# Kernel tuning notes

Measured on AMD Instinct MI355X. Metric: run time of the kernel, lower is better.

The kernel has to match this reference:

```python
import jax, jax.numpy as jnp
import numpy as np

NUM_ITERS = 3
NUM_SLOTS = 8
D = 128
MLP_HIDDEN = 128
EPS = 1e-8
LN_EPS = 1e-5
B, N = 64, 4096


def _layer_norm(x, g, b):
    m = jnp.mean(x, axis=-1, keepdims=True)
    v = jnp.mean(jnp.square(x - m), axis=-1, keepdims=True)
    return (x - m) * jax.lax.rsqrt(v + LN_EPS) * g + b


def setup_inputs() -> dict:
    key = jax.random.key(0)
    ks = jax.random.split(key, 16)
    s = 1.0 / np.sqrt(D)
    inp = {
        "x": jax.random.normal(ks[0], (B, N, D), jnp.float32),
        "slots_init": jax.random.normal(ks[1], (B, NUM_SLOTS, D), jnp.float32),
        "Wq": jax.random.normal(ks[2], (D, D), jnp.float32) * s,
        "bq": jnp.zeros((D,), jnp.float32),
        "Wk": jax.random.normal(ks[3], (D, D), jnp.float32) * s,
        "bk": jnp.zeros((D,), jnp.float32),
        "Wv": jax.random.normal(ks[4], (D, D), jnp.float32) * s,
        "bv": jnp.zeros((D,), jnp.float32),
        "g_in": jnp.ones((D,), jnp.float32), "b_in": jnp.zeros((D,), jnp.float32),
        "g_slot": jnp.ones((D,), jnp.float32), "b_slot": jnp.zeros((D,), jnp.float32),
        "g_mlp": jnp.ones((D,), jnp.float32), "b_mlp": jnp.zeros((D,), jnp.float32),
        "W1": jax.random.normal(ks[5], (MLP_HIDDEN, D), jnp.float32) * s,
        "b1": jnp.zeros((MLP_HIDDEN,), jnp.float32),
        "W2": jax.random.normal(ks[6], (D, MLP_HIDDEN), jnp.float32) * (1.0 / np.sqrt(MLP_HIDDEN)),
        "b2": jnp.zeros((D,), jnp.float32),
        "W_ih": jax.random.normal(ks[7], (3 * D, D), jnp.float32) * s,
        "W_hh": jax.random.normal(ks[8], (3 * D, D), jnp.float32) * s,
        "b_ih": jnp.zeros((3 * D,), jnp.float32),
        "b_hh": jnp.zeros((3 * D,), jnp.float32),
    }
    return inp


def _gru_cell(x, h, W_ih, W_hh, b_ih, b_hh):
    # torch.nn.GRUCell semantics
    gi = x @ W_ih.T + b_ih          # [.., 3D]
    gh = h @ W_hh.T + b_hh
    i_r, i_z, i_n = jnp.split(gi, 3, axis=-1)
    h_r, h_z, h_n = jnp.split(gh, 3, axis=-1)
    r = jax.nn.sigmoid(i_r + h_r)
    z = jax.nn.sigmoid(i_z + h_z)
    n = jnp.tanh(i_n + r * h_n)
    return (1.0 - z) * n + z * h


def reference(x, slots_init, Wq, bq, Wk, bk, Wv, bv, g_in, b_in, g_slot, b_slot,
              g_mlp, b_mlp, W1, b1, W2, b2, W_ih, W_hh, b_ih, b_hh):
    xn = _layer_norm(x, g_in, b_in)                 # [B,N,D]
    keys = xn @ Wk.T + bk                            # [B,N,D]
    values = xn @ Wv.T + bv                          # [B,N,D]
    scale = D ** -0.5
    slots = slots_init                               # [B,K,D]
    for _ in range(NUM_ITERS):
        prev = slots
        s = _layer_norm(slots, g_slot, b_slot)
        q = s @ Wq.T + bq                            # [B,K,D]
        logits = jnp.einsum('bid,bkd->bik', q, keys) * scale  # [B,K,N]
        attn = jax.nn.softmax(logits, axis=1)        # softmax over SLOT axis
        attn = attn + EPS
        attn = attn / jnp.sum(attn, axis=-1, keepdims=True)
        updates = jnp.einsum('bkd,bik->bid', values, attn)     # [B,K,D]
        slots = _gru_cell(updates.reshape(-1, D), prev.reshape(-1, D),
                          W_ih, W_hh, b_ih, b_hh).reshape(x.shape[0], -1, D)
        h = jax.nn.relu(_layer_norm(slots, g_mlp, b_mlp) @ W1.T + b1)
        slots = slots + (h @ W2.T + b2)
    return slots
```

## Files before the change

### kernel.cpp

```cpp
#include <hip/hip_runtime.h>
#include <hip/hip_bf16.h>

#define B_ 64
#define N_ 4096
#define KS 8
#define NCH 32
#define NG 2
#define TP 136
#define LNEPS 1e-5f
#define EPSA 1e-8f
#define SCALE 0.08838834764831845f

typedef short short8  __attribute__((ext_vector_type(8)));
typedef short short4v __attribute__((ext_vector_type(4)));
typedef float f32x4   __attribute__((ext_vector_type(4)));

__device__ __forceinline__ unsigned short f2bf(float f) {
  union { float f; unsigned u; } v; v.f = f;
  unsigned r = v.u + 0x7fffu + ((v.u >> 16) & 1u);
  return (unsigned short)(r >> 16);
}
__device__ __forceinline__ float bflo(unsigned u) {
  union { unsigned u; float f; } c; c.u = u << 16; return c.f;
}
__device__ __forceinline__ float bfhi(unsigned u) {
  union { unsigned u; float f; } c; c.u = u & 0xffff0000u; return c.f;
}
__device__ __forceinline__ float sigmf(float x) { return 1.f / (1.f + __expf(-x)); }

__global__ __launch_bounds__(256) void prep_weights(
    const float* __restrict__ Wih, const float* __restrict__ Whh,
    const float* __restrict__ Wq,  const float* __restrict__ Wv,
    const float* __restrict__ W1,  const float* __restrict__ W2,
    float* __restrict__ WgT, float* __restrict__ WqT,
    float* __restrict__ WvT, float* __restrict__ W1T, float* __restrict__ W2T)
{
  int id = blockIdx.x * 256 + threadIdx.x;
  if (id < 98304) {
    int d = id / 768, j = id % 768;
    WgT[id] = (j < 384) ? Wih[j*128 + d] : Whh[(j-384)*128 + d];
  } else if (id < 114688) {
    int k = id - 98304; WqT[k] = Wq[(k % 128) * 128 + k / 128];
  } else if (id < 131072) {
    int k = id - 114688; WvT[k] = Wv[(k % 128) * 128 + k / 128];
  } else if (id < 147456) {
    int k = id - 131072; W1T[k] = W1[(k % 128) * 128 + k / 128];
  } else if (id < 163840) {
    int k = id - 147456; W2T[k] = W2[(k % 128) * 128 + k / 128];
  }
}

__global__ __launch_bounds__(256) void q_init_kernel(
    const float* __restrict__ slots_in, const float* __restrict__ g_slot, const float* __restrict__ b_slot,
    const float* __restrict__ WqT, const float* __restrict__ bq,
    const float* __restrict__ Wk, const float* __restrict__ bk,
    float* __restrict__ qt, float* __restrict__ qc)
{
  __shared__ float sarr[128];
  __shared__ float qarr[128];
  int row = blockIdx.x, t = threadIdx.x;
  if (t < 64) {
    float a = slots_in[row*128 + t], b = slots_in[row*128 + 64 + t];
    float s = a + b, s2 = a*a + b*b;
    #pragma unroll
    for (int st = 1; st < 64; st <<= 1) { s += __shfl_xor(s, st); s2 += __shfl_xor(s2, st); }
    float mean = s * (1.f/128.f);
    float rstd = rsqrtf(s2 * (1.f/128.f) - mean*mean + LNEPS);
    sarr[t]    = (a - mean) * rstd * g_slot[t]    + b_slot[t];
    sarr[t+64] = (b - mean) * rstd * g_slot[t+64] + b_slot[t+64];
  }
  __syncthreads();
  if (t < 128) {
    float a = bq[t];
    for (int d = 0; d < 128; d++) a += sarr[d] * WqT[d*128 + t];
    qarr[t] = a;
  }
  __syncthreads();
  if (t < 128) {
    float a = 0.f;
    for (int j = 0; j < 128; j++) a += qarr[j] * Wk[j*128 + t];
    qt[row*128 + t] = a * SCALE;
  }
  if (t < 64) {
    float c = qarr[t]*bk[t] + qarr[t+64]*bk[t+64];
    #pragma unroll
    for (int st = 1; st < 64; st <<= 1) c += __shfl_xor(c, st);
    if (t == 0) qc[row] = c * SCALE;
  }
}

__global__ __launch_bounds__(256) void ln_kernel(
    const float* __restrict__ x, const float* __restrict__ g_in, const float* __restrict__ b_in,
    unsigned short* __restrict__ xn)
{
  const int tid = threadIdx.x;
  const int w = tid >> 6, lane = tid & 63;
  const int half = lane >> 5, sl = lane & 31;
  const size_t row0 = (size_t)blockIdx.x * 128 + w * 32 + half;

  float4 gg = *(const float4*)(g_in + sl*4);
  float4 bb = *(const float4*)(b_in + sl*4);

  for (int i = 0; i < 16; i++) {
    size_t row = row0 + i*2;
    float4 v = *(const float4*)(x + row*128 + sl*4);
    float s  = v.x + v.y + v.z + v.w;
    float s2 = v.x*v.x + v.y*v.y + v.z*v.z + v.w*v.w;
    #pragma unroll
    for (int st = 1; st < 32; st <<= 1) { s += __shfl_xor(s, st); s2 += __shfl_xor(s2, st); }
    float mean = s * (1.f/128.f);
    float rstd = rsqrtf(s2*(1.f/128.f) - mean*mean + LNEPS);
    unsigned short h0 = f2bf((v.x - mean)*rstd*gg.x + bb.x);
    unsigned short h1 = f2bf((v.y - mean)*rstd*gg.y + bb.y);
    unsigned short h2 = f2bf((v.z - mean)*rstd*gg.z + bb.z);
    unsigned short h3 = f2bf((v.w - mean)*rstd*gg.w + bb.w);
    uint2 pk;
    pk.x = (unsigned)h0 | ((unsigned)h1 << 16);
    pk.y = (unsigned)h2 | ((unsigned)h3 << 16);
    *(uint2*)(xn + row*128 + sl*4) = pk;
  }
}

__global__ __launch_bounds__(256) void attn_kernel(
    unsigned short* __restrict__ xn,
    const float* __restrict__ qt, const float* __restrict__ qc,
    float* __restrict__ Upart, float* __restrict__ Spart)
{
  __shared__ union ShMem {
    unsigned short xt[4][16][TP];
    float ured[4][8][128];
  } sh;
  __shared__ __align__(16) float pb[4][16][8];
  __shared__ float sred[4][8];

  const int tid = threadIdx.x;
  const int w = tid >> 6, lane = tid & 63;
  const int chunk = blockIdx.x, batch = blockIdx.y;
  const int m = lane & 15, quad = lane >> 4;

  short8 afrag[4];
  if (m < KS) {
    const float* qp = qt + (batch*KS + m)*128 + quad*8;
    #pragma unroll
    for (int kc = 0; kc < 4; kc++) {
      short8 a;
      #pragma unroll
      for (int j = 0; j < 8; j++) a[j] = (short)f2bf(qp[kc*32 + j]);
      afrag[kc] = a;
    }
  } else {
    #pragma unroll
    for (int kc = 0; kc < 4; kc++) {
      short8 a;
      #pragma unroll
      for (int j = 0; j < 8; j++) a[j] = 0;
      afrag[kc] = a;
    }
  }
  float creg[4];
  #pragma unroll
  for (int r = 0; r < 4; r++) creg[r] = qc[batch*KS + ((quad*4 + r) & 7)];

  float u0[8], u1[8];
  #pragma unroll
  for (int i = 0; i < 8; i++) { u0[i] = 0.f; u1[i] = 0.f; }
  float sAcc[4] = {0.f, 0.f, 0.f, 0.f};

  for (int g = 0; g < NG; g++) {
    const int tb = ((chunk*4 + w)*NG + g)*16;

    short8 bfrag[4];
    const unsigned short* xp = xn + (size_t)(batch*N_ + tb + m)*128;
    #pragma unroll
    for (int kc = 0; kc < 4; kc++) {
      bfrag[kc] = *(const short8*)(xp + kc*32 + quad*8);
      *(short8*)&sh.xt[w][m][kc*32 + quad*8] = bfrag[kc];
    }

    f32x4 acc = {0.f, 0.f, 0.f, 0.f};
    #pragma unroll
    for (int kc = 0; kc < 4; kc++)
      acc = __builtin_amdgcn_mfma_f32_16x16x32_bf16(afrag[kc], bfrag[kc], acc, 0, 0, 0);
    float l[4], o[4];
    #pragma unroll
    for (int r = 0; r < 4; r++) l[r] = acc[r] + creg[r];
    #pragma unroll
    for (int r = 0; r < 4; r++) o[r] = __shfl_xor(l[r], 16);
    float mx = fmaxf(fmaxf(fmaxf(l[0], l[1]), fmaxf(l[2], l[3])),
                     fmaxf(fmaxf(o[0], o[1]), fmaxf(o[2], o[3])));
    float e0 = __expf(l[0]-mx), e1 = __expf(l[1]-mx), e2 = __expf(l[2]-mx), e3 = __expf(l[3]-mx);
    float den = e0+e1+e2+e3 + __expf(o[0]-mx)+__expf(o[1]-mx)+__expf(o[2]-mx)+__expf(o[3]-mx);
    float rd = 1.f / den;
    float p0 = e0*rd + EPSA, p1 = e1*rd + EPSA, p2 = e2*rd + EPSA, p3 = e3*rd + EPSA;
    if (lane < 32) {
      float4 pv; pv.x = p0; pv.y = p1; pv.z = p2; pv.w = p3;
      *(float4*)&pb[w][m][quad*4] = pv;
    }

    #pragma unroll
    for (int t = 0; t < 16; t++) {
      float4 pA = *(const float4*)&pb[w][t][0];
      float4 pB = *(const float4*)&pb[w][t][4];
      unsigned vp = *(const unsigned*)&sh.xt[w][t][lane*2];
      float f0 = bflo(vp), f1 = bfhi(vp);
      u0[0] += pA.x*f0; u1[0] += pA.x*f1;
      u0[1] += pA.y*f0; u1[1] += pA.y*f1;
      u0[2] += pA.z*f0; u1[2] += pA.z*f1;
      u0[3] += pA.w*f0; u1[3] += pA.w*f1;
      u0[4] += pB.x*f0; u1[4] += pB.x*f1;
      u0[5] += pB.y*f0; u1[5] += pB.y*f1;
      u0[6] += pB.z*f0; u1[6] += pB.z*f1;
      u0[7] += pB.w*f0; u1[7] += pB.w*f1;
    }

    float sac[4] = {p0, p1, p2, p3};
    #pragma unroll
    for (int st = 1; st < 16; st <<= 1) {
      #pragma unroll
      for (int r = 0; r < 4; r++) sac[r] += __shfl_xor(sac[r], st);
    }
    #pragma unroll
    for (int r = 0; r < 4; r++) sAcc[r] += sac[r];
  }

  if (lane == 0)  { sred[w][0]=sAcc[0]; sred[w][1]=sAcc[1]; sred[w][2]=sAcc[2]; sred[w][3]=sAcc[3]; }
  if (lane == 16) { sred[w][4]=sAcc[0]; sred[w][5]=sAcc[1]; sred[w][6]=sAcc[2]; sred[w][7]=sAcc[3]; }

  __syncthreads();
  #pragma unroll
  for (int i = 0; i < 8; i++)
    *(float2*)&sh.ured[w][i][lane*2] = make_float2(u0[i], u1[i]);
  __syncthreads();

  {
    const float* ur = &sh.ured[0][0][0];
    int i4 = tid * 4;
    float4 a = *(const float4*)(ur + i4);
    float4 b = *(const float4*)(ur + 1024 + i4);
    float4 c = *(const float4*)(ur + 2048 + i4);
    float4 d = *(const float4*)(ur + 3072 + i4);
    float4 o4;
    o4.x = a.x+b.x+c.x+d.x; o4.y = a.y+b.y+c.y+d.y;
    o4.z = a.z+b.z+c.z+d.z; o4.w = a.w+b.w+c.w+d.w;
    *(float4*)(Upart + (size_t)(batch*NCH + chunk)*1024 + i4) = o4;
    if (tid < 8)
      Spart[(batch*NCH + chunk)*8 + tid] =
        sred[0][tid] + sred[1][tid] + sred[2][tid] + sred[3][tid];
  }
}

__global__ __launch_bounds__(256) void update_kernel(
    const float* __restrict__ slots_in, float* __restrict__ slots_out,
    const float* __restrict__ Upart, const float* __restrict__ Spart,
    const float* __restrict__ WvT, const float* __restrict__ bv,
    const float* __restrict__ WgT,
    const float* __restrict__ b_ih, const float* __restrict__ b_hh,
    const float* __restrict__ g_mlp, const float* __restrict__ b_mlp,
    const float* __restrict__ W1T, const float* __restrict__ b1,
    const float* __restrict__ W2T, const float* __restrict__ b2,
    const float* __restrict__ g_slot, const float* __restrict__ b_slot,
    const float* __restrict__ WqT, const float* __restrict__ bq,
    const float* __restrict__ Wk, const float* __restrict__ bk,
    float* __restrict__ qt, float* __restrict__ qc)
{
  __shared__ float bu[128], su[128], hb[128];
  __shared__ float gg[768];
  __shared__ float s1[128], smv[128], hmv[128], s2v[128], sqv[128], qa[128];
  __shared__ float up2[2][128];
  __shared__ float stats[2], sSum;
  int row = blockIdx.x, t = threadIdx.x;
  int batch = row >> 3, slot = row & 7;
  const int col = t & 127, hf = t >> 7;

  {
    const float* Up = Upart + ((size_t)(batch*NCH + hf*16)*8 + slot)*128 + col;
    float ua = 0.f;
    #pragma unroll
    for (int c = 0; c < 16; c++) ua += Up[(size_t)c*1024];
    up2[hf][col] = ua;
  }
  if (t < NCH) {
    float sv = Spart[(batch*NCH + t)*8 + slot];
    #pragma unroll
    for (int st = 1; st < NCH; st <<= 1) sv += __shfl_xor(sv, st);
    if (t == 0) sSum = sv;
  }
  if (t >= 64 && t < 192) hb[t-64] = slots_in[row*128 + (t-64)];
  __syncthreads();
  if (t < 128) bu[t] = (up2[0][t] + up2[1][t]) / sSum;
  __syncthreads();
  {
    float a = hf ? 0.f : bv[col];
    const float* W = WvT + hf*64*128;
    const float* v = bu + hf*64;
    #pragma unroll 8
    for (int d = 0; d < 64; d++) a += v[d] * W[d*128 + col];
    __syncthreads();
    up2[hf][col] = a;
  }
  __syncthreads();
  if (t < 128) su[t] = up2[0][t] + up2[1][t];
  __syncthreads();
  {
    float a0 = b_ih[t];
    float a1 = (t < 128) ? b_ih[256+t] : b_hh[t-128];
    float a2 = b_hh[t+128];
    const float* v1p = (t < 128) ? su : hb;
    for (int d = 0; d < 128; d++) {
      float sd = su[d], hd = hb[d], vd = v1p[d];
      const float* wr = WgT + d*768 + t;
      a0 += sd * wr[0];
      a1 += vd * wr[256];
      a2 += hd * wr[512];
    }
    gg[t] = a0; gg[t+256] = a1; gg[t+512] = a2;
  }
  __syncthreads();
  if (t < 128) {
    float r = sigmf(gg[t] + gg[384+t]);
    float z = sigmf(gg[128+t] + gg[512+t]);
    float n = tanhf(gg[256+t] + r * gg[640+t]);
    s1[t] = (1.f - z)*n + z*hb[t];
  }
  __syncthreads();
  if (t < 64) {
    float a = s1[t], b = s1[t+64];
    float s = a + b, s2 = a*a + b*b;
    #pragma unroll
    for (int st = 1; st < 64; st <<= 1) { s += __shfl_xor(s, st); s2 += __shfl_xor(s2, st); }
    if (t == 0) { float mean = s*(1.f/128.f); stats[0] = mean;
                  stats[1] = rsqrtf(s2*(1.f/128.f) - mean*mean + LNEPS); }
  }
  __syncthreads();
  if (t < 128) smv[t] = (s1[t] - stats[0])*stats[1]*g_mlp[t] + b_mlp[t];
  __syncthreads();
  {
    float a = hf ? 0.f : b1[col];
    const float* W = W1T + hf*64*128;
    const float* v = smv + hf*64;
    #pragma unroll 8
    for (int d = 0; d < 64; d++) a += v[d] * W[d*128 + col];
    up2[hf][col] = a;
  }
  __syncthreads();
  if (t < 128) hmv[t] = fmaxf(up2[0][t] + up2[1][t], 0.f);
  __syncthreads();
  {
    float a = 0.f;
    const float* W = W2T + hf*64*128;
    const float* v = hmv + hf*64;
    #pragma unroll 8
    for (int d = 0; d < 64; d++) a += v[d] * W[d*128 + col];
    up2[hf][col] = a;
  }
  __syncthreads();
  if (t < 128) {
    float a = s1[t] + b2[t] + up2[0][t] + up2[1][t];
    s2v[t] = a;
    slots_out[row*128 + t] = a;
  }
  __syncthreads();
  if (t < 64) {
    float a = s2v[t], b = s2v[t+64];
    float s = a + b, s2 = a*a + b*b;
    #pragma unroll
    for (int st = 1; st < 64; st <<= 1) { s += __shfl_xor(s, st); s2 += __shfl_xor(s2, st); }
    if (t == 0) { float mean = s*(1.f/128.f); stats[0] = mean;
                  stats[1] = rsqrtf(s2*(1.f/128.f) - mean*mean + LNEPS); }
  }
  __syncthreads();
  if (t < 128) sqv[t] = (s2v[t] - stats[0])*stats[1]*g_slot[t] + b_slot[t];
  __syncthreads();
  {
    float a = hf ? 0.f : bq[col];
    const float* W = WqT + hf*64*128;
    const float* v = sqv + hf*64;
    #pragma unroll 8
    for (int d = 0; d < 64; d++) a += v[d] * W[d*128 + col];
    up2[hf][col] = a;
  }
  __syncthreads();
  if (t < 128) qa[t] = up2[0][t] + up2[1][t];
  __syncthreads();
  {
    float a = 0.f;
    const float* W = Wk + hf*64*128;
    const float* v = qa + hf*64;
    #pragma unroll 8
    for (int j = 0; j < 64; j++) a += v[j] * W[j*128 + col];
    up2[hf][col] = a;
  }
  __syncthreads();
  if (t < 128) qt[row*128 + t] = (up2[0][t] + up2[1][t]) * SCALE;
  if (t < 64) {
    float c = qa[t]*bk[t] + qa[t+64]*bk[t+64];
    #pragma unroll
    for (int st = 1; st < 64; st <<= 1) c += __shfl_xor(c, st);
    if (t == 0) qc[row] = c * SCALE;
  }
}

extern "C" void kernel_launch(void* const* d_in, const int* in_sizes, int n_in,
                              void* d_out, int out_size, void* d_ws, size_t ws_size,
                              hipStream_t stream) {
  const float* x          = (const float*)d_in[0];
  const float* slots_init = (const float*)d_in[1];
  const float* Wq   = (const float*)d_in[2];
  const float* bq   = (const float*)d_in[3];
  const float* Wk   = (const float*)d_in[4];
  const float* bk   = (const float*)d_in[5];
  const float* Wv   = (const float*)d_in[6];
  const float* bv   = (const float*)d_in[7];
  const float* g_in = (const float*)d_in[8];
  const float* b_in = (const float*)d_in[9];
  const float* g_slot = (const float*)d_in[10];
  const float* b_slot = (const float*)d_in[11];
  const float* g_mlp  = (const float*)d_in[12];
  const float* b_mlp  = (const float*)d_in[13];
  const float* W1   = (const float*)d_in[14];
  const float* b1   = (const float*)d_in[15];
  const float* W2   = (const float*)d_in[16];
  const float* b2   = (const float*)d_in[17];
  const float* Wih  = (const float*)d_in[18];
  const float* Whh  = (const float*)d_in[19];
  const float* b_ih = (const float*)d_in[20];
  const float* b_hh = (const float*)d_in[21];

  char* p = (char*)d_ws;
  unsigned short* xn = (unsigned short*)p; p += (size_t)B_*N_*128*2;
  float* qt    = (float*)p; p += (size_t)B_*KS*128*4;
  float* qc    = (float*)p; p += (size_t)B_*KS*4 + 2048;
  float* slots = (float*)p; p += (size_t)B_*KS*128*4;
  float* Upart = (float*)p; p += (size_t)B_*NCH*KS*128*4;
  float* Spart = (float*)p; p += (size_t)B_*NCH*KS*4 + 2048;
  float* WgT   = (float*)p; p += 98304*4;
  float* WqT   = (float*)p; p += 16384*4;
  float* WvT   = (float*)p; p += 16384*4;
  float* W1T   = (float*)p; p += 16384*4;
  float* W2T   = (float*)p; p += 16384*4;

  prep_weights<<<640, 256, 0, stream>>>(Wih, Whh, Wq, Wv, W1, W2,
                                        WgT, WqT, WvT, W1T, W2T);
  q_init_kernel<<<512, 256, 0, stream>>>(slots_init, g_slot, b_slot, WqT, bq, Wk, bk, qt, qc);

  ln_kernel<<<2048, 256, 0, stream>>>(x, g_in, b_in, xn);

  attn_kernel<<<dim3(NCH, B_), 256, 0, stream>>>(xn, qt, qc, Upart, Spart);
  update_kernel<<<512, 256, 0, stream>>>(slots_init, slots, Upart, Spart,
      WvT, bv, WgT, b_ih, b_hh, g_mlp, b_mlp, W1T, b1, W2T, b2,
      g_slot, b_slot, WqT, bq, Wk, bk, qt, qc);

  attn_kernel<<<dim3(NCH, B_), 256, 0, stream>>>(xn, qt, qc, Upart, Spart);
  update_kernel<<<512, 256, 0, stream>>>(slots, slots, Upart, Spart,
      WvT, bv, WgT, b_ih, b_hh, g_mlp, b_mlp, W1T, b1, W2T, b2,
      g_slot, b_slot, WqT, bq, Wk, bk, qt, qc);

  attn_kernel<<<dim3(NCH, B_), 256, 0, stream>>>(xn, qt, qc, Upart, Spart);
  update_kernel<<<512, 256, 0, stream>>>(slots, (float*)d_out, Upart, Spart,
      WvT, bv, WgT, b_ih, b_hh, g_mlp, b_mlp, W1T, b1, W2T, b2,
      g_slot, b_slot, WqT, bq, Wk, bk, qt, qc);

  (void)in_sizes; (void)n_in; (void)out_size; (void)ws_size;
}
```

Measured before the change: 395.8 us.

## Merge prep, q-init and layernorm kernels; prefetch tiles and use packed FMA

```diff
diff --git a/kernel.cpp b/kernel.cpp
--- a/kernel.cpp
+++ b/kernel.cpp
@@ -5,7 +5,6 @@
 #define N_ 4096
 #define KS 8
 #define NCH 32
-#define NG 2
 #define TP 136
 #define LNEPS 1e-5f
 #define EPSA 1e-8f
@@ -14,6 +13,7 @@
 typedef short short8  __attribute__((ext_vector_type(8)));
 typedef short short4v __attribute__((ext_vector_type(4)));
 typedef float f32x4   __attribute__((ext_vector_type(4)));
+typedef float f32x2   __attribute__((ext_vector_type(2)));
 
 __device__ __forceinline__ unsigned short f2bf(float f) {
   union { float f; unsigned u; } v; v.f = f;
@@ -28,101 +28,109 @@
 }
 __device__ __forceinline__ float sigmf(float x) { return 1.f / (1.f + __expf(-x)); }
 
-__global__ __launch_bounds__(256) void prep_weights(
+__device__ __forceinline__ void pkfma_lo(f32x2 &d, f32x2 f, f32x2 p2) {
+  asm("v_pk_fma_f32 %0, %1, %2, %0 op_sel_hi:[1,0,1]" : "+v"(d) : "v"(f), "v"(p2));
+}
+__device__ __forceinline__ void pkfma_hi(f32x2 &d, f32x2 f, f32x2 p2) {
+  asm("v_pk_fma_f32 %0, %1, %2, %0 op_sel:[0,1,0] op_sel_hi:[1,1,1]" : "+v"(d) : "v"(f), "v"(p2));
+}
+
+__global__ __launch_bounds__(256) void prep_all(
     const float* __restrict__ Wih, const float* __restrict__ Whh,
     const float* __restrict__ Wq,  const float* __restrict__ Wv,
     const float* __restrict__ W1,  const float* __restrict__ W2,
     float* __restrict__ WgT, float* __restrict__ WqT,
-    float* __restrict__ WvT, float* __restrict__ W1T, float* __restrict__ W2T)
-{
-  int id = blockIdx.x * 256 + threadIdx.x;
-  if (id < 98304) {
-    int d = id / 768, j = id % 768;
-    WgT[id] = (j < 384) ? Wih[j*128 + d] : Whh[(j-384)*128 + d];
-  } else if (id < 114688) {
-    int k = id - 98304; WqT[k] = Wq[(k % 128) * 128 + k / 128];
-  } else if (id < 131072) {
-    int k = id - 114688; WvT[k] = Wv[(k % 128) * 128 + k / 128];
-  } else if (id < 147456) {
-    int k = id - 131072; W1T[k] = W1[(k % 128) * 128 + k / 128];
-  } else if (id < 163840) {
-    int k = id - 147456; W2T[k] = W2[(k % 128) * 128 + k / 128];
-  }
-}
-
-__global__ __launch_bounds__(256) void q_init_kernel(
+    float* __restrict__ WvT, float* __restrict__ W1T, float* __restrict__ W2T,
     const float* __restrict__ slots_in, const float* __restrict__ g_slot, const float* __restrict__ b_slot,
-    const float* __restrict__ WqT, const float* __restrict__ bq,
+    const float* __restrict__ bq,
     const float* __restrict__ Wk, const float* __restrict__ bk,
-    float* __restrict__ qt, float* __restrict__ qc)
+    float* __restrict__ qt, float* __restrict__ qc,
+    const float* __restrict__ x, const float* __restrict__ g_in, const float* __restrict__ b_in,
+    unsigned short* __restrict__ xn)
 {
   __shared__ float sarr[128];
   __shared__ float qarr[128];
-  int row = blockIdx.x, t = threadIdx.x;
-  if (t < 64) {
-    float a = slots_in[row*128 + t], b = slots_in[row*128 + 64 + t];
-    float s = a + b, s2 = a*a + b*b;
-    #pragma unroll
-    for (int st = 1; st < 64; st <<= 1) { s += __shfl_xor(s, st); s2 += __shfl_xor(s2, st); }
-    float mean = s * (1.f/128.f);
-    float rstd = rsqrtf(s2 * (1.f/128.f) - mean*mean + LNEPS);
-    sarr[t]    = (a - mean) * rstd * g_slot[t]    + b_slot[t];
-    sarr[t+64] = (b - mean) * rstd * g_slot[t+64] + b_slot[t+64];
-  }
-  __syncthreads();
-  if (t < 128) {
-    float a = bq[t];
-    for (int d = 0; d < 128; d++) a += sarr[d] * WqT[d*128 + t];
-    qarr[t] = a;
-  }
-  __syncthreads();
-  if (t < 128) {
-    float a = 0.f;
-    for (int j = 0; j < 128; j++) a += qarr[j] * Wk[j*128 + t];
-    qt[row*128 + t] = a * SCALE;
-  }
-  if (t < 64) {
-    float c = qarr[t]*bk[t] + qarr[t+64]*bk[t+64];
-    #pragma unroll
-    for (int st = 1; st < 64; st <<= 1) c += __shfl_xor(c, st);
-    if (t == 0) qc[row] = c * SCALE;
-  }
-}
-
-__global__ __launch_bounds__(256) void ln_kernel(
-    const float* __restrict__ x, const float* __restrict__ g_in, const float* __restrict__ b_in,
-    unsigned short* __restrict__ xn)
-{
-  const int tid = threadIdx.x;
-  const int w = tid >> 6, lane = tid & 63;
-  const int half = lane >> 5, sl = lane & 31;
-  const size_t row0 = (size_t)blockIdx.x * 128 + w * 32 + half;
-
-  float4 gg = *(const float4*)(g_in + sl*4);
-  float4 bb = *(const float4*)(b_in + sl*4);
-
-  for (int i = 0; i < 16; i++) {
-    size_t row = row0 + i*2;
-    float4 v = *(const float4*)(x + row*128 + sl*4);
-    float s  = v.x + v.y + v.z + v.w;
-    float s2 = v.x*v.x + v.y*v.y + v.z*v.z + v.w*v.w;
-    #pragma unroll
-    for (int st = 1; st < 32; st <<= 1) { s += __shfl_xor(s, st); s2 += __shfl_xor(s2, st); }
-    float mean = s * (1.f/128.f);
-    float rstd = rsqrtf(s2*(1.f/128.f) - mean*mean + LNEPS);
-    unsigned short h0 = f2bf((v.x - mean)*rstd*gg.x + bb.x);
-    unsigned short h1 = f2bf((v.y - mean)*rstd*gg.y + bb.y);
-    unsigned short h2 = f2bf((v.z - mean)*rstd*gg.z + bb.z);
-    unsigned short h3 = f2bf((v.w - mean)*rstd*gg.w + bb.w);
-    uint2 pk;
-    pk.x = (unsigned)h0 | ((unsigned)h1 << 16);
-    pk.y = (unsigned)h2 | ((unsigned)h3 << 16);
-    *(uint2*)(xn + row*128 + sl*4) = pk;
+  const int bb = blockIdx.x, t = threadIdx.x;
+
+  if (bb < 640) {
+    int id = bb * 256 + t;
+    if (id < 98304) {
+      int d = id / 768, j = id % 768;
+      WgT[id] = (j < 384) ? Wih[j*128 + d] : Whh[(j-384)*128 + d];
+    } else if (id < 114688) {
+      int k = id - 98304; WqT[k] = Wq[(k % 128) * 128 + k / 128];
+    } else if (id < 131072) {
+      int k = id - 114688; WvT[k] = Wv[(k % 128) * 128 + k / 128];
+    } else if (id < 147456) {
+      int k = id - 131072; W1T[k] = W1[(k % 128) * 128 + k / 128];
+    } else if (id < 163840) {
+      int k = id - 147456; W2T[k] = W2[(k % 128) * 128 + k / 128];
+    }
+    return;
+  }
+
+  if (bb < 1152) {
+    int row = bb - 640;
+    if (t < 64) {
+      float a = slots_in[row*128 + t], b = slots_in[row*128 + 64 + t];
+      float s = a + b, s2 = a*a + b*b;
+      #pragma unroll
+      for (int st = 1; st < 64; st <<= 1) { s += __shfl_xor(s, st); s2 += __shfl_xor(s2, st); }
+      float mean = s * (1.f/128.f);
+      float rstd = rsqrtf(s2 * (1.f/128.f) - mean*mean + LNEPS);
+      sarr[t]    = (a - mean) * rstd * g_slot[t]    + b_slot[t];
+      sarr[t+64] = (b - mean) * rstd * g_slot[t+64] + b_slot[t+64];
+    }
+    __syncthreads();
+    if (t < 128) {
+      float a = bq[t];
+      for (int d = 0; d < 128; d++) a += sarr[d] * Wq[t*128 + d];
+      qarr[t] = a;
+    }
+    __syncthreads();
+    if (t < 128) {
+      float a = 0.f;
+      for (int j = 0; j < 128; j++) a += qarr[j] * Wk[j*128 + t];
+      qt[row*128 + t] = a * SCALE;
+    }
+    if (t < 64) {
+      float c = qarr[t]*bk[t] + qarr[t+64]*bk[t+64];
+      #pragma unroll
+      for (int st = 1; st < 64; st <<= 1) c += __shfl_xor(c, st);
+      if (t == 0) qc[row] = c * SCALE;
+    }
+    return;
+  }
+
+  {
+    const int w = t >> 6, lane = t & 63;
+    const int half = lane >> 5, sl = lane & 31;
+    const size_t row0 = (size_t)(bb - 1152) * 128 + w * 32 + half;
+    float4 gg = *(const float4*)(g_in + sl*4);
+    float4 bv4 = *(const float4*)(b_in + sl*4);
+    for (int i = 0; i < 16; i++) {
+      size_t row = row0 + i*2;
+      float4 v = *(const float4*)(x + row*128 + sl*4);
+      float s  = v.x + v.y + v.z + v.w;
+      float s2 = v.x*v.x + v.y*v.y + v.z*v.z + v.w*v.w;
+      #pragma unroll
+      for (int st = 1; st < 32; st <<= 1) { s += __shfl_xor(s, st); s2 += __shfl_xor(s2, st); }
+      float mean = s * (1.f/128.f);
+      float rstd = rsqrtf(s2*(1.f/128.f) - mean*mean + LNEPS);
+      unsigned short h0 = f2bf((v.x - mean)*rstd*gg.x + bv4.x);
+      unsigned short h1 = f2bf((v.y - mean)*rstd*gg.y + bv4.y);
+      unsigned short h2 = f2bf((v.z - mean)*rstd*gg.z + bv4.z);
+      unsigned short h3 = f2bf((v.w - mean)*rstd*gg.w + bv4.w);
+      uint2 pk;
+      pk.x = (unsigned)h0 | ((unsigned)h1 << 16);
+      pk.y = (unsigned)h2 | ((unsigned)h3 << 16);
+      *(uint2*)(xn + row*128 + sl*4) = pk;
+    }
   }
 }
 
 __global__ __launch_bounds__(256) void attn_kernel(
-    unsigned short* __restrict__ xn,
+    const unsigned short* __restrict__ xn,
     const float* __restrict__ qt, const float* __restrict__ qc,
     float* __restrict__ Upart, float* __restrict__ Spart)
 {
@@ -161,26 +169,32 @@
   #pragma unroll
   for (int r = 0; r < 4; r++) creg[r] = qc[batch*KS + ((quad*4 + r) & 7)];
 
-  float u0[8], u1[8];
-  #pragma unroll
-  for (int i = 0; i < 8; i++) { u0[i] = 0.f; u1[i] = 0.f; }
+  const int tb = (chunk*4 + w) * 32;
+  const unsigned short* xp0 = xn + (size_t)(batch*N_ + tb + m)*128;
+  const unsigned short* xp1 = xp0 + 16*128;
+  short8 bfA[4], bfB[4];
+  #pragma unroll
+  for (int kc = 0; kc < 4; kc++) bfA[kc] = *(const short8*)(xp0 + kc*32 + quad*8);
+  #pragma unroll
+  for (int kc = 0; kc < 4; kc++) bfB[kc] = *(const short8*)(xp1 + kc*32 + quad*8);
+
+  f32x2 u01[8];
+  #pragma unroll
+  for (int i = 0; i < 8; i++) { u01[i].x = 0.f; u01[i].y = 0.f; }
   float sAcc[4] = {0.f, 0.f, 0.f, 0.f};
 
-  for (int g = 0; g < NG; g++) {
-    const int tb = ((chunk*4 + w)*NG + g)*16;
-
-    short8 bfrag[4];
-    const unsigned short* xp = xn + (size_t)(batch*N_ + tb + m)*128;
-    #pragma unroll
-    for (int kc = 0; kc < 4; kc++) {
-      bfrag[kc] = *(const short8*)(xp + kc*32 + quad*8);
-      *(short8*)&sh.xt[w][m][kc*32 + quad*8] = bfrag[kc];
-    }
+  #pragma unroll
+  for (int g = 0; g < 2; g++) {
+    short8* bf = g ? bfB : bfA;
+
+    #pragma unroll
+    for (int kc = 0; kc < 4; kc++)
+      *(short8*)&sh.xt[w][m][kc*32 + quad*8] = bf[kc];
 
     f32x4 acc = {0.f, 0.f, 0.f, 0.f};
     #pragma unroll
     for (int kc = 0; kc < 4; kc++)
-      acc = __builtin_amdgcn_mfma_f32_16x16x32_bf16(afrag[kc], bfrag[kc], acc, 0, 0, 0);
+      acc = __builtin_amdgcn_mfma_f32_16x16x32_bf16(afrag[kc], bf[kc], acc, 0, 0, 0);
     float l[4], o[4];
     #pragma unroll
     for (int r = 0; r < 4; r++) l[r] = acc[r] + creg[r];
@@ -199,18 +213,16 @@
 
     #pragma unroll
     for (int t = 0; t < 16; t++) {
-      float4 pA = *(const float4*)&pb[w][t][0];
-      float4 pB = *(const float4*)&pb[w][t][4];
+      f32x2 pA01 = *(const f32x2*)&pb[w][t][0];
+      f32x2 pA23 = *(const f32x2*)&pb[w][t][2];
+      f32x2 pB01 = *(const f32x2*)&pb[w][t][4];
+      f32x2 pB23 = *(const f32x2*)&pb[w][t][6];
       unsigned vp = *(const unsigned*)&sh.xt[w][t][lane*2];
-      float f0 = bflo(vp), f1 = bfhi(vp);
-      u0[0] += pA.x*f0; u1[0] += pA.x*f1;
-      u0[1] += pA.y*f0; u1[1] += pA.y*f1;
-      u0[2] += pA.z*f0; u1[2] += pA.z*f1;
-      u0[3] += pA.w*f0; u1[3] += pA.w*f1;
-      u0[4] += pB.x*f0; u1[4] += pB.x*f1;
-      u0[5] += pB.y*f0; u1[5] += pB.y*f1;
-      u0[6] += pB.z*f0; u1[6] += pB.z*f1;
-      u0[7] += pB.w*f0; u1[7] += pB.w*f1;
+      f32x2 f; f.x = bflo(vp); f.y = bfhi(vp);
+      pkfma_lo(u01[0], f, pA01); pkfma_hi(u01[1], f, pA01);
+      pkfma_lo(u01[2], f, pA23); pkfma_hi(u01[3], f, pA23);
+      pkfma_lo(u01[4], f, pB01); pkfma_hi(u01[5], f, pB01);
+      pkfma_lo(u01[6], f, pB23); pkfma_hi(u01[7], f, pB23);
     }
 
     float sac[4] = {p0, p1, p2, p3};
@@ -229,7 +241,7 @@
   __syncthreads();
   #pragma unroll
   for (int i = 0; i < 8; i++)
-    *(float2*)&sh.ured[w][i][lane*2] = make_float2(u0[i], u1[i]);
+    *(f32x2*)&sh.ured[w][i][lane*2] = u01[i];
   __syncthreads();
 
   {
@@ -439,11 +451,10 @@
   float* W1T   = (float*)p; p += 16384*4;
   float* W2T   = (float*)p; p += 16384*4;
 
-  prep_weights<<<640, 256, 0, stream>>>(Wih, Whh, Wq, Wv, W1, W2,
-                                        WgT, WqT, WvT, W1T, W2T);
-  q_init_kernel<<<512, 256, 0, stream>>>(slots_init, g_slot, b_slot, WqT, bq, Wk, bk, qt, qc);
-
-  ln_kernel<<<2048, 256, 0, stream>>>(x, g_in, b_in, xn);
+  prep_all<<<3200, 256, 0, stream>>>(Wih, Whh, Wq, Wv, W1, W2,
+      WgT, WqT, WvT, W1T, W2T,
+      slots_init, g_slot, b_slot, bq, Wk, bk, qt, qc,
+      x, g_in, b_in, xn);
 
   attn_kernel<<<dim3(NCH, B_), 256, 0, stream>>>(xn, qt, qc, Upart, Spart);
   update_kernel<<<512, 256, 0, stream>>>(slots_init, slots, Upart, Spart,
```

Result: faster. 377.0 us (-4.8%).
